# Optimization experiments

Measured on AMD Instinct MI355X. Metric: run time of the kernel, lower is better.

Reference implementation:

```python
import jax, jax.numpy as jnp
import numpy as np

V_THRESHOLD = 1.0
V_RESET = 0.0
TAU = 2.0
SURROGATE_PARAM = 0.5  # 'zo' (rectangular window) surrogate half-width


@jax.custom_vjp
def act_fun(x):
    # Heaviside step: spike if membrane exceeds threshold
    return (x > 0).astype(x.dtype)


def _act_fwd(x):
    return act_fun(x), x


def _act_bwd(x, g):
    # zero-order / rectangular surrogate gradient:
    # d spike / dx = 1/(2a) * 1[|x| < a]
    a = SURROGATE_PARAM
    grad = g * (jnp.abs(x) < a).astype(g.dtype) / (2.0 * a)
    return (grad,)


act_fun.defvjp(_act_fwd, _act_bwd)


def lif_forward(X):
    # X: [B, T, N] -> spikes [B, T, N]
    Xt = jnp.swapaxes(X, 0, 1)  # [T, B, N]

    def step(mem, x_t):
        # leaky integration toward (input + v_reset)
        mem = mem + (x_t + V_RESET - mem) / TAU
        spike = act_fun(mem - V_THRESHOLD)
        # hard reset to v_reset where spiked
        mem = (1.0 - spike) * mem + V_RESET * spike
        return mem, spike

    mem0 = jnp.zeros(Xt.shape[1:], dtype=X.dtype)
    _, spikes = jax.lax.scan(step, mem0, Xt)  # spikes: [T, B, N]
    return jnp.swapaxes(spikes, 0, 1)  # [B, T, N]


def setup_inputs() -> dict:
    key = jax.random.key(0)
    B, T, N = 128, 32, 8192
    X = jax.random.normal(key, (B, T, N), dtype=jnp.float32)
    return {"X": X}


def reference(X):
    return lif_forward(X)
```

## Files before the change

kernel.cpp:

```cpp
#include <hip/hip_runtime.h>


#define T_STEPS 32
#define N2 4096
#define TN2 (T_STEPS * N2)

__global__ __launch_bounds__(256) void lif_fwd_kernel(
    const float2* __restrict__ X, float2* __restrict__ out)
{
    const int idx = blockIdx.x * blockDim.x + threadIdx.x;
    const int b = idx >> 12;
    const int n = idx & (N2 - 1);
    const size_t base = (size_t)b * (size_t)TN2 + (size_t)n;

    const float2* p = X + base;
    float2* __restrict__ po = out + base;

    float2 x[T_STEPS];
#pragma unroll
    for (int t = 0; t < T_STEPS; ++t) {
        asm volatile("global_load_dwordx2 %0, %1, off"
                     : "=v"(x[t])
                     : "v"(p));
        p += N2;
    }

    asm volatile("s_waitcnt vmcnt(0)" ::: "memory");

#pragma unroll
    for (int t = 0; t < T_STEPS; ++t)
        asm volatile("" : "+v"(x[t]));

    float m0 = 0.f, m1 = 0.f;
#pragma unroll
    for (int t = 0; t < T_STEPS; ++t) {
        m0 = m0 + (x[t].x - m0) * 0.5f;
        m1 = m1 + (x[t].y - m1) * 0.5f;

        float2 s;
        s.x = (m0 - 1.0f > 0.0f) ? 1.0f : 0.0f;
        s.y = (m1 - 1.0f > 0.0f) ? 1.0f : 0.0f;

        m0 = (s.x != 0.0f) ? 0.0f : m0;
        m1 = (s.y != 0.0f) ? 0.0f : m1;

        po[(size_t)t * (size_t)N2] = s;
    }
}

extern "C" void kernel_launch(void* const* d_in, const int* in_sizes, int n_in,
                              void* d_out, int out_size, void* d_ws, size_t ws_size,
                              hipStream_t stream) {
    const float2* X = (const float2*)d_in[0];
    float2* out = (float2*)d_out;

    const int total = in_sizes[0];
    const int B = total / (T_STEPS * 8192);
    const int nthreads = B * N2;

    const int block = 256;
    const int grid = (nthreads + block - 1) / block;

    lif_fwd_kernel<<<grid, block, 0, stream>>>(X, out);
}
```

Before: 223.9 us.

## Widen loads to 128-bit and process time steps in two 16-step batches

Each thread now handles four neurons using 128-bit vector loads and stores, halving the thread count. The 32 time-step loads are split into two batches of 16 with a wait between them, and launch bounds request higher occupancy. The goal is fewer, wider memory transactions and lower register pressure per thread. The trade-off is that the mid-kernel wait serialises the two load batches, which may reduce memory-level parallelism.

```diff
diff --git a/kernel.cpp b/kernel.cpp
--- a/kernel.cpp
+++ b/kernel.cpp
@@ -1,62 +1,74 @@
 #include <hip/hip_runtime.h>
 
 
+typedef float f32x4 __attribute__((ext_vector_type(4)));
+
 #define T_STEPS 32
-#define N2 4096
-#define TN2 (T_STEPS * N2)
+#define N4 2048
+#define TN4 (T_STEPS * N4)
 
-__global__ __launch_bounds__(256) void lif_fwd_kernel(
-    const float2* __restrict__ X, float2* __restrict__ out)
+__global__ __launch_bounds__(256, 4) void lif_fwd_kernel(
+    const f32x4* __restrict__ X, f32x4* __restrict__ out)
 {
     const int idx = blockIdx.x * blockDim.x + threadIdx.x;
-    const int b = idx >> 12;
-    const int n = idx & (N2 - 1);
-    const size_t base = (size_t)b * (size_t)TN2 + (size_t)n;
+    const int b = idx >> 11;
+    const int n = idx & (N4 - 1);
+    const size_t base = (size_t)b * (size_t)TN4 + (size_t)n;
 
-    const float2* p = X + base;
-    float2* __restrict__ po = out + base;
+    const f32x4* p = X + base;
+    f32x4* __restrict__ po = out + base;
 
-    float2 x[T_STEPS];
-#pragma unroll
-    for (int t = 0; t < T_STEPS; ++t) {
-        asm volatile("global_load_dwordx2 %0, %1, off"
-                     : "=v"(x[t])
-                     : "v"(p));
-        p += N2;
-    }
-
-    asm volatile("s_waitcnt vmcnt(0)" ::: "memory");
+    float m0 = 0.f, m1 = 0.f, m2 = 0.f, m3 = 0.f;
+    f32x4 x[16];
 
 #pragma unroll
-    for (int t = 0; t < T_STEPS; ++t)
-        asm volatile("" : "+v"(x[t]));
+    for (int half = 0; half < 2; ++half) {
+#pragma unroll
+        for (int t = 0; t < 16; ++t) {
+            asm volatile("global_load_dwordx4 %0, %1, off"
+                         : "=&v"(x[t])
+                         : "v"(p));
+            p += N4;
+        }
 
-    float m0 = 0.f, m1 = 0.f;
+        asm volatile("s_waitcnt vmcnt(0)" ::: "memory");
+
 #pragma unroll
-    for (int t = 0; t < T_STEPS; ++t) {
-        m0 = m0 + (x[t].x - m0) * 0.5f;
-        m1 = m1 + (x[t].y - m1) * 0.5f;
+        for (int t = 0; t < 16; ++t)
+            asm volatile("" : "+v"(x[t]));
 
-        float2 s;
-        s.x = (m0 - 1.0f > 0.0f) ? 1.0f : 0.0f;
-        s.y = (m1 - 1.0f > 0.0f) ? 1.0f : 0.0f;
+#pragma unroll
+        for (int t = 0; t < 16; ++t) {
+            m0 = m0 + (x[t].x - m0) * 0.5f;
+            m1 = m1 + (x[t].y - m1) * 0.5f;
+            m2 = m2 + (x[t].z - m2) * 0.5f;
+            m3 = m3 + (x[t].w - m3) * 0.5f;
 
-        m0 = (s.x != 0.0f) ? 0.0f : m0;
-        m1 = (s.y != 0.0f) ? 0.0f : m1;
+            f32x4 s;
+            s.x = (m0 - 1.0f > 0.0f) ? 1.0f : 0.0f;
+            s.y = (m1 - 1.0f > 0.0f) ? 1.0f : 0.0f;
+            s.z = (m2 - 1.0f > 0.0f) ? 1.0f : 0.0f;
+            s.w = (m3 - 1.0f > 0.0f) ? 1.0f : 0.0f;
 
-        po[(size_t)t * (size_t)N2] = s;
+            m0 = (s.x != 0.0f) ? 0.0f : m0;
+            m1 = (s.y != 0.0f) ? 0.0f : m1;
+            m2 = (s.z != 0.0f) ? 0.0f : m2;
+            m3 = (s.w != 0.0f) ? 0.0f : m3;
+
+            po[(size_t)(half * 16 + t) * (size_t)N4] = s;
+        }
     }
 }
 
 extern "C" void kernel_launch(void* const* d_in, const int* in_sizes, int n_in,
                               void* d_out, int out_size, void* d_ws, size_t ws_size,
                               hipStream_t stream) {
-    const float2* X = (const float2*)d_in[0];
-    float2* out = (float2*)d_out;
+    const f32x4* X = (const f32x4*)d_in[0];
+    f32x4* out = (f32x4*)d_out;
 
     const int total = in_sizes[0];
     const int B = total / (T_STEPS * 8192);
-    const int nthreads = B * N2;
+    const int nthreads = B * N4;
 
     const int block = 256;
     const int grid = (nthreads + block - 1) / block;
```

Result: slower. 233.6 us (+4.4%).
